# Kernel optimization log

Hardware: AMD Instinct MI355X
Metric: run time of the kernel (lower is better)

The kernel has to match this reference:

```python
import jax, jax.numpy as jnp
import numpy as np

B, NJ, NM = 64, 30, 20
N = NJ * NM          # 600 operation nodes per FJSP instance
IN_DIM, H = 2, 128


def _bn(h):
    # torch BatchNorm1d in training mode, gamma=1/beta=0 (module init), stats over all nodes
    m = h.mean(axis=(0, 1))
    v = h.var(axis=(0, 1))
    return (h - m) / jnp.sqrt(v + 1e-5)


def setup_inputs() -> dict:
    key = jax.random.key(0)
    ks = jax.random.split(key, 20)
    x = jax.random.normal(ks[0], (B, N, IN_DIM), jnp.float32)
    graph_pool = jnp.full((B, N), 1.0 / N, jnp.float32)   # average graph pooling weights
    padded_nei = jnp.zeros((1,), jnp.int32)               # unused (sum pooling path)
    adj = (jax.random.uniform(ks[1], (B, N, N)) < 0.01).astype(jnp.float32)
    adj = jnp.minimum(adj + jnp.eye(N, dtype=jnp.float32)[None], 1.0)  # self-loops
    candidate = jax.random.randint(ks[2], (B, NJ), 0, N)
    a_index = jax.random.randint(ks[3], (B,), 0, NJ)
    mask = jax.random.uniform(ks[4], (B, NJ)) < 0.2
    mask = mask.at[jnp.arange(B), a_index].set(False)     # chosen action never masked
    mask_mch = jax.random.uniform(ks[5], (B, N, NM)) < 0.3
    dur = jax.random.uniform(ks[6], (B, N, NM), dtype=jnp.float32)
    old_action = jax.random.randint(ks[7], (B,), 0, N)
    mch_pool = jax.random.normal(ks[8], (B, H), jnp.float32)

    def w(k, i, o):
        return jax.random.normal(k, (i, o), jnp.float32) * (1.0 / np.sqrt(i))

    z = lambda n: jnp.zeros((n,), jnp.float32)            # biases init to 0 in module
    return dict(
        x=x, graph_pool=graph_pool, padded_nei=padded_nei, adj=adj,
        candidate=candidate, mask=mask, mask_mch=mask_mch, dur=dur,
        a_index=a_index, old_action=old_action, mch_pool=mch_pool,
        W1_0=w(ks[9], IN_DIM, H), b1_0=z(H), W2_0=w(ks[10], H, H), b2_0=z(H),
        W1_1=w(ks[11], H, H), b1_1=z(H), W2_1=w(ks[12], H, H), b2_1=z(H),
        Wa1=w(ks[13], 3 * H, H), ba1=z(H), Wa2=w(ks[14], H, H), ba2=z(H),
        Wa3=w(ks[15], H, 1), ba3=z(1),
        Wc1=w(ks[16], H, H), bc1=z(H), Wc2=w(ks[17], H, 1), bc2=z(1),
    )


def reference(x, graph_pool, padded_nei, adj, candidate, mask, mask_mch, dur,
              a_index, old_action, mch_pool,
              W1_0, b1_0, W2_0, b2_0, W1_1, b1_1, W2_1, b2_1,
              Wa1, ba1, Wa2, ba2, Wa3, ba3, Wc1, bc1, Wc2, bc2):
    # --- GIN encoder: num_layers-1 = 2 message-passing layers, sum pooling ---
    h = x
    for (W1, b1, W2, b2) in ((W1_0, b1_0, W2_0, b2_0), (W1_1, b1_1, W2_1, b2_1)):
        pooled = jnp.einsum('bnm,bmd->bnd', adj, h)         # neighbor sum (adj has self-loops)
        h1 = jax.nn.relu(_bn(pooled @ W1 + b1))             # MLP hidden (BN inside MLP)
        h = jax.nn.relu(_bn(h1 @ W2 + b2))                  # layer BN + relu
    h_nodes = h                                             # [B, N, H]
    h_pooled = jnp.einsum('bn,bnd->bd', graph_pool, h_nodes)  # [B, H]

    # --- gather candidate features, concat pooled contexts ---
    cand_feat = jnp.take_along_axis(h_nodes, candidate[:, :, None], axis=1)  # [B, NJ, H]
    concat = jnp.concatenate([
        cand_feat,
        jnp.broadcast_to(h_pooled[:, None, :], cand_feat.shape),
        jnp.broadcast_to(mch_pool[:, None, :], cand_feat.shape)], axis=-1)   # [B, NJ, 3H]

    # --- MLPActor(3 layers, tanh) ---
    a = jnp.tanh(concat @ Wa1 + ba1)
    a = jnp.tanh(a @ Wa2 + ba2)
    scores = (a @ Wa3 + ba3).squeeze(-1) * 10.0             # [B, NJ]
    scores = jnp.where(mask, -jnp.inf, scores)
    logpi = jax.nn.log_softmax(scores, axis=1)
    pi = jnp.exp(logpi)
    log_a = jnp.take_along_axis(logpi, a_index[:, None], axis=1)[:, 0]
    entropy = -jnp.sum(jnp.where(pi > 0, pi * logpi, 0.0), axis=1)

    # --- gather action-dependent tensors (detached in torch) ---
    b_idx = jnp.arange(B)
    action_node = dur[b_idx, old_action]                    # [B, NM]
    action_feature = h_nodes[b_idx, old_action]             # [B, H]
    mask_mch_action = mask_mch[b_idx, old_action][:, None, :]  # [B, 1, NM]

    # --- MLPCritic(2 layers, tanh) ---
    v = jnp.tanh(h_pooled @ Wc1 + bc1) @ Wc2 + bc2          # [B, 1]

    sg = jax.lax.stop_gradient
    return (entropy, v, log_a, sg(action_node), sg(action_feature),
            mask_mch_action, sg(h_pooled))
```

## Files before the change

### kernel.cpp

```cpp
#include <hip/hip_runtime.h>
#include <hip/hip_bf16.h>

#define BB 64
#define NJ 30
#define NM 20
#define NN 600
#define HH 128
#define NROWS (BB*NN)
#define CAP 48

typedef __attribute__((ext_vector_type(8))) short short8;
typedef __attribute__((ext_vector_type(4))) float f32x4;

#define STATS_B   0
#define HPOOL_B   4096
#define FLAGS_B   36864
#define ZERO_B    36880
#define WTB_B     37120
#define SCORES_B  135424
#define NBRCNT_B  143104
#define NBRIDX_B  296704
#define POOLED0_B 7669504
#define T1_B      7976704
#define P1_B      27637504

#define OUT_ENT   0
#define OUT_V     64
#define OUT_LOGA  128
#define OUT_ANODE 192
#define OUT_AFEAT 1472
#define OUT_MMCH  9664
#define OUT_HPOOL 10944

__device__ __forceinline__ bool mask_at(const void* p, int layout, long i) {
    if (layout == 2) return ((const float*)p)[i] != 0.f;
    if (layout == 1) return ((const unsigned char*)p)[i] != 0;
    return ((const int*)p)[i] != 0;
}

__device__ __forceinline__ short bf16rne(float f) {
    unsigned u = __float_as_uint(f);
    return (short)((u + 0x7fffu + ((u >> 16) & 1u)) >> 16);
}
__device__ __forceinline__ float bf2f(unsigned h) {
    return __uint_as_float(h << 16);
}
__device__ __forceinline__ unsigned packbf(float a, float b) {
    return ((unsigned)(unsigned short)bf16rne(a)) |
           (((unsigned)(unsigned short)bf16rne(b)) << 16);
}

__global__ __launch_bounds__(256) void k_detect(const void* mask_p, const void* maskmch_p,
                                                int* flags) {
    unsigned agg = 0;
    int which;
    int tid = threadIdx.x;
    if (blockIdx.x == 0) {
        which = 0;
        const unsigned* p = (const unsigned*)mask_p;
        unsigned w0 = (tid < 480) ? p[tid] : 0u;
        unsigned w1 = (tid + 256 < 480) ? p[tid + 256] : 0u;
        agg = w0 | w1;
    } else {
        which = 1;
        const unsigned* p = (const unsigned*)maskmch_p + (size_t)(blockIdx.x - 1) * 800;
        unsigned w0 = p[tid];
        unsigned w1 = (tid + 256 < 800) ? p[tid + 256] : 0u;
        unsigned w2 = (tid + 512 < 800) ? p[tid + 512] : 0u;
        unsigned w3 = (tid + 768 < 800) ? p[tid + 768] : 0u;
        agg = w0 | w1 | w2 | w3;
    }
    int f = 0;
    if (((agg >> 24) & 0xffu) == 0x3fu) f |= 1;
    if ((((agg >> 8) & 0xffu) == 1u) || (((agg >> 16) & 0xffu) == 1u) ||
        (((agg >> 24) & 0xffu) == 1u)) f |= 2;
#pragma unroll
    for (int off = 1; off < 64; off <<= 1) f |= __shfl_xor(f, off);
    if ((tid & 63) == 0 && f) atomicOr(&flags[which], f);
}

__global__ void k_wconv(const float* __restrict__ Wa, const float* __restrict__ Wb,
                        const float* __restrict__ Wc, unsigned short* __restrict__ wT) {
    int mat = blockIdx.x >> 6;
    int idx = ((blockIdx.x & 63) << 8) + threadIdx.x;
    const float* W = mat == 0 ? Wa : (mat == 1 ? Wb : Wc);
    int k = idx >> 7, c = idx & 127;
    wT[mat * 16384 + c * HH + k] = (unsigned short)bf16rne(W[idx]);
}

__global__ __launch_bounds__(256) void k_sparse(const float* __restrict__ adj,
                                                const float* __restrict__ x,
                                                int* __restrict__ nbr_cnt,
                                                int* __restrict__ nbr_idx,
                                                float* __restrict__ pooled0) {
    int wrow = blockIdx.x * 4 + (threadIdx.x >> 6);
    int lane = threadIdx.x & 63;
    int b = wrow / NN;
    const float4* arow = (const float4*)(adj + (size_t)wrow * NN);
    int* irow = nbr_idx + (size_t)wrow * CAP;
    const float* xb = x + (size_t)b * NN * 2;
    float4 vv[3];
    vv[0] = arow[lane];
    vv[1] = arow[64 + lane];
    vv[2] = (128 + lane < 150) ? arow[128 + lane] : make_float4(0.f, 0.f, 0.f, 0.f);
    int cnt = 0;
    float p0 = 0.f, p1 = 0.f;
#pragma unroll
    for (int it = 0; it < 3; ++it) {
        int fi = it * 64 + lane;
#pragma unroll
        for (int s = 0; s < 4; ++s) {
            float c = s == 0 ? vv[it].x : (s == 1 ? vv[it].y : (s == 2 ? vv[it].z : vv[it].w));
            bool pred = (c != 0.f);
            unsigned long long bal = __ballot(pred);
            if (pred) {
                int pos = cnt + __popcll(bal & ((1ull << lane) - 1ull));
                int m = fi * 4 + s;
                if (pos < CAP) irow[pos] = m;
                float2 xv = *(const float2*)&xb[m * 2];
                p0 += xv.x; p1 += xv.y;
            }
            cnt += __popcll(bal);
        }
    }
#pragma unroll
    for (int off = 1; off < 64; off <<= 1) {
        p0 += __shfl_xor(p0, off);
        p1 += __shfl_xor(p1, off);
    }
    if (lane == 0) {
        nbr_cnt[wrow] = cnt < CAP ? cnt : CAP;
        pooled0[(size_t)wrow * 2]     = p0;
        pooled0[(size_t)wrow * 2 + 1] = p1;
    }
}

__global__ __launch_bounds__(256) void k_p0stats(const float* __restrict__ pooled0,
                                                 float* __restrict__ out5) {
    __shared__ float red[4][5];
    int i = blockIdx.x * 256 + threadIdx.x;
    float p0 = pooled0[(size_t)i * 2], p1 = pooled0[(size_t)i * 2 + 1];
    float v[5] = {p0, p1, p0 * p0, p1 * p1, p0 * p1};
#pragma unroll
    for (int j = 0; j < 5; ++j)
#pragma unroll
        for (int off = 1; off < 64; off <<= 1) v[j] += __shfl_xor(v[j], off);
    int lane = threadIdx.x & 63, w = threadIdx.x >> 6;
    if (lane == 0)
#pragma unroll
        for (int j = 0; j < 5; ++j) red[w][j] = v[j];
    __syncthreads();
    if (threadIdx.x == 0)
#pragma unroll
        for (int j = 0; j < 5; ++j)
            atomicAdd(&out5[j], red[0][j] + red[1][j] + red[2][j] + red[3][j]);
}

template<int MODE>
__global__ __launch_bounds__(256) void k_stage(const void* __restrict__ t_in_v,
                                               const float* __restrict__ pooled0,
                                               const float* __restrict__ W1,
                                               const unsigned short* __restrict__ wT,
                                               const float* __restrict__ stats_in,
                                               unsigned short* __restrict__ t_out,
                                               float* __restrict__ stats_out) {
    __shared__ float sm_mean[HH], sm_inv[HH];
    __shared__ float smS[4][HH], smQ[4][HH];
    int tid = threadIdx.x;
    if (MODE == 0 && tid < HH) {
        float S0 = stats_in[0], S1 = stats_in[1], Q0 = stats_in[2], Q1 = stats_in[3], P01 = stats_in[4];
        float w0 = W1[tid], w1 = W1[HH + tid];
        float m = (S0 * w0 + S1 * w1) * (1.f / NROWS);
        float eq = (Q0 * w0 * w0 + Q1 * w1 * w1 + 2.f * P01 * w0 * w1) * (1.f / NROWS);
        sm_mean[tid] = m;
        sm_inv[tid] = 1.f / sqrtf(eq - m * m + 1e-5f);
    }
    if (MODE == 1 && tid < HH) {
        float s = stats_in[tid], q = stats_in[HH + tid];
        float m = s * (1.f / NROWS);
        sm_mean[tid] = m;
        sm_inv[tid] = 1.f / sqrtf(q * (1.f / NROWS) - m * m + 1e-5f);
    }
    if (MODE != 2) __syncthreads();

    const unsigned short* tin = (const unsigned short*)t_in_v;
    int lane = tid & 63, wave = tid >> 6;
    int r16 = lane & 15, kg = lane >> 4;
    int rowbase = blockIdx.x * 64 + wave * 16;

    f32x4 acc[8];
#pragma unroll
    for (int t = 0; t < 8; ++t)
#pragma unroll
        for (int i = 0; i < 4; ++i) acc[t][i] = 0.f;

    float p0 = 0.f, p1 = 0.f;
    if (MODE == 0) {
        p0 = pooled0[(size_t)(rowbase + r16) * 2];
        p1 = pooled0[(size_t)(rowbase + r16) * 2 + 1];
    }

#pragma unroll
    for (int ks = 0; ks < 4; ++ks) {
        int kb = ks * 32 + kg * 8;
        short8 afr;
        if (MODE == 2) {
            afr = *(const short8*)&tin[(size_t)(rowbase + r16) * HH + kb];
        } else {
            float av[8];
            if (MODE == 0) {
                float4 wa0 = *(const float4*)&W1[kb];
                float4 wa1 = *(const float4*)&W1[kb + 4];
                float4 wb0 = *(const float4*)&W1[HH + kb];
                float4 wb1 = *(const float4*)&W1[HH + kb + 4];
                av[0] = p0 * wa0.x + p1 * wb0.x; av[1] = p0 * wa0.y + p1 * wb0.y;
                av[2] = p0 * wa0.z + p1 * wb0.z; av[3] = p0 * wa0.w + p1 * wb0.w;
                av[4] = p0 * wa1.x + p1 * wb1.x; av[5] = p0 * wa1.y + p1 * wb1.y;
                av[6] = p0 * wa1.z + p1 * wb1.z; av[7] = p0 * wa1.w + p1 * wb1.w;
            } else {
                short8 raw = *(const short8*)&tin[(size_t)(rowbase + r16) * HH + kb];
#pragma unroll
                for (int j = 0; j < 8; ++j) av[j] = bf2f((unsigned short)raw[j]);
            }
            float4 m0 = *(const float4*)&sm_mean[kb];
            float4 m1 = *(const float4*)&sm_mean[kb + 4];
            float4 i0 = *(const float4*)&sm_inv[kb];
            float4 i1 = *(const float4*)&sm_inv[kb + 4];
            av[0] = fmaxf((av[0] - m0.x) * i0.x, 0.f);
            av[1] = fmaxf((av[1] - m0.y) * i0.y, 0.f);
            av[2] = fmaxf((av[2] - m0.z) * i0.z, 0.f);
            av[3] = fmaxf((av[3] - m0.w) * i0.w, 0.f);
            av[4] = fmaxf((av[4] - m1.x) * i1.x, 0.f);
            av[5] = fmaxf((av[5] - m1.y) * i1.y, 0.f);
            av[6] = fmaxf((av[6] - m1.z) * i1.z, 0.f);
            av[7] = fmaxf((av[7] - m1.w) * i1.w, 0.f);
#pragma unroll
            for (int j = 0; j < 8; ++j) afr[j] = bf16rne(av[j]);
        }
#pragma unroll
        for (int t = 0; t < 8; ++t) {
            short8 bfr = *(const short8*)&wT[(size_t)(t * 16 + r16) * HH + kb];
            acc[t] = __builtin_amdgcn_mfma_f32_16x16x32_bf16(afr, bfr, acc[t], 0, 0, 0);
        }
    }

#pragma unroll
    for (int t = 0; t < 8; ++t) {
        int col = t * 16 + r16;
        float s = 0.f, q = 0.f;
#pragma unroll
        for (int i = 0; i < 4; ++i) {
            float v = acc[t][i];
            t_out[(size_t)(rowbase + kg * 4 + i) * HH + col] = (unsigned short)bf16rne(v);
            s += v; q += v * v;
        }
        s += __shfl_xor(s, 16); q += __shfl_xor(q, 16);
        s += __shfl_xor(s, 32); q += __shfl_xor(q, 32);
        if (kg == 0) { smS[wave][col] = s; smQ[wave][col] = q; }
    }
    __syncthreads();
    if (tid < HH) {
        atomicAdd(&stats_out[tid],      smS[0][tid] + smS[1][tid] + smS[2][tid] + smS[3][tid]);
        atomicAdd(&stats_out[HH + tid], smQ[0][tid] + smQ[1][tid] + smQ[2][tid] + smQ[3][tid]);
    }
}

__global__ __launch_bounds__(256) void k_pool1(const unsigned short* __restrict__ t1,
                                               const int* __restrict__ nbr_cnt,
                                               const int* __restrict__ nbr_idx,
                                               const float* __restrict__ stats1,
                                               unsigned short* __restrict__ pooled1) {
    __shared__ float sm_mean[HH], sm_inv[HH];
    int tid = threadIdx.x;
    if (tid < HH) {
        float s = stats1[tid], q = stats1[HH + tid];
        float m = s * (1.f / NROWS);
        sm_mean[tid] = m;
        sm_inv[tid] = 1.f / sqrtf(q * (1.f / NROWS) - m * m + 1e-5f);
    }
    __syncthreads();
    int c4 = tid & 31, rl = tid >> 5;
    int row = blockIdx.x * 8 + rl;
    int b = row / NN;
    float4 mm = *(const float4*)&sm_mean[c4 * 4];
    float4 iv = *(const float4*)&sm_inv[c4 * 4];
    int cnt = nbr_cnt[row];
    const int* ir = nbr_idx + (size_t)row * CAP;
    const unsigned short* tb = t1 + (size_t)b * NN * HH;
    float a0 = 0.f, a1 = 0.f, a2 = 0.f, a3 = 0.f;
    int i = 0;
    for (; i + 1 < cnt; i += 2) {
        int m0 = ir[i], m1 = ir[i + 1];
        uint2 w0 = *(const uint2*)&tb[(size_t)m0 * HH + c4 * 4];
        uint2 w1 = *(const uint2*)&tb[(size_t)m1 * HH + c4 * 4];
        a0 += fmaxf((bf2f(w0.x & 0xffffu) - mm.x) * iv.x, 0.f)
            + fmaxf((bf2f(w1.x & 0xffffu) - mm.x) * iv.x, 0.f);
        a1 += fmaxf((bf2f(w0.x >> 16)     - mm.y) * iv.y, 0.f)
            + fmaxf((bf2f(w1.x >> 16)     - mm.y) * iv.y, 0.f);
        a2 += fmaxf((bf2f(w0.y & 0xffffu) - mm.z) * iv.z, 0.f)
            + fmaxf((bf2f(w1.y & 0xffffu) - mm.z) * iv.z, 0.f);
        a3 += fmaxf((bf2f(w0.y >> 16)     - mm.w) * iv.w, 0.f)
            + fmaxf((bf2f(w1.y >> 16)     - mm.w) * iv.w, 0.f);
    }
    if (i < cnt) {
        int m0 = ir[i];
        uint2 w0 = *(const uint2*)&tb[(size_t)m0 * HH + c4 * 4];
        a0 += fmaxf((bf2f(w0.x & 0xffffu) - mm.x) * iv.x, 0.f);
        a1 += fmaxf((bf2f(w0.x >> 16)     - mm.y) * iv.y, 0.f);
        a2 += fmaxf((bf2f(w0.y & 0xffffu) - mm.z) * iv.z, 0.f);
        a3 += fmaxf((bf2f(w0.y >> 16)     - mm.w) * iv.w, 0.f);
    }
    uint2 o;
    o.x = packbf(a0, a1);
    o.y = packbf(a2, a3);
    *(uint2*)&pooled1[(size_t)row * HH + c4 * 4] = o;
}

__global__ __launch_bounds__(256) void k_hpool(const unsigned short* __restrict__ t3,
                                               const float* __restrict__ gp,
                                               const float* __restrict__ stats3,
                                               float* __restrict__ hpool) {
    __shared__ float sm_mean[HH], sm_inv[HH];
    __shared__ float red[256];
    int tid = threadIdx.x;
    if (tid < HH) {
        float s = stats3[tid], q = stats3[HH + tid];
        float m = s * (1.f / NROWS);
        sm_mean[tid] = m;
        sm_inv[tid] = 1.f / sqrtf(q * (1.f / NROWS) - m * m + 1e-5f);
    }
    __syncthreads();
    int b = blockIdx.x >> 3, chunk = blockIdx.x & 7;
    int c = tid & 127, rr = tid >> 7;
    float m = sm_mean[c], iv = sm_inv[c];
    float acc = 0.f;
    for (int n = chunk * 75 + rr; n < chunk * 75 + 75; n += 2) {
        float w = gp[b * NN + n];
        float v = bf2f(t3[((size_t)b * NN + n) * HH + c]);
        acc += w * fmaxf((v - m) * iv, 0.f);
    }
    red[tid] = acc;
    __syncthreads();
    if (tid < HH) atomicAdd(&hpool[b * HH + c], red[c] + red[c + 128]);
}

__global__ __launch_bounds__(256) void k_actor(const unsigned short* __restrict__ t3,
                                               const int* __restrict__ cand,
                                               const float* __restrict__ hpool,
                                               const float* __restrict__ mch,
                                               const float* __restrict__ stats3,
                                               const float* __restrict__ Wa1,
                                               const float* __restrict__ ba1,
                                               const float* __restrict__ Wa2,
                                               const float* __restrict__ ba2,
                                               const float* __restrict__ Wa3,
                                               const float* __restrict__ ba3,
                                               float* __restrict__ scores) {
    __shared__ float sh_c[8 * 384];
    __shared__ float sh_a1[8 * HH];
    __shared__ float sred[8][HH];
    int tid = threadIdx.x;
    int rbase = blockIdx.x * 8;
    int c = tid & 127, slot = tid >> 7;

    float mean_c, inv_c;
    {
        float s = stats3[c], q = stats3[HH + c];
        float m = s * (1.f / NROWS);
        mean_c = m;
        inv_c = 1.f / sqrtf(q * (1.f / NROWS) - m * m + 1e-5f);
    }
#pragma unroll
    for (int rr = 0; rr < 4; ++rr) {
        int r = slot * 4 + rr;
        int row = rbase + r;
        int b = row / NJ;
        int cd = cand[row];
        float v = bf2f(t3[((size_t)b * NN + cd) * HH + c]);
        sh_c[r * 384 + c]       = fmaxf((v - mean_c) * inv_c, 0.f);
        sh_c[r * 384 + 128 + c] = hpool[b * HH + c];
        sh_c[r * 384 + 256 + c] = mch[b * HH + c];
    }
    __syncthreads();

    float acc[4] = {0.f, 0.f, 0.f, 0.f};
    for (int k = 0; k < 384; ++k) {
        float w = Wa1[(size_t)k * HH + c];
#pragma unroll
        for (int rr = 0; rr < 4; ++rr)
            acc[rr] += sh_c[(slot * 4 + rr) * 384 + k] * w;
    }
    float bb = ba1[c];
#pragma unroll
    for (int rr = 0; rr < 4; ++rr)
        sh_a1[(slot * 4 + rr) * HH + c] = tanhf(acc[rr] + bb);
    __syncthreads();

    float acc2[4] = {0.f, 0.f, 0.f, 0.f};
    for (int k = 0; k < HH; ++k) {
        float w = Wa2[(size_t)k * HH + c];
#pragma unroll
        for (int rr = 0; rr < 4; ++rr)
            acc2[rr] += sh_a1[(slot * 4 + rr) * HH + k] * w;
    }
    float w3 = Wa3[c], bb2 = ba2[c];
#pragma unroll
    for (int rr = 0; rr < 4; ++rr)
        sred[slot * 4 + rr][c] = tanhf(acc2[rr] + bb2) * w3;
    __syncthreads();
    int r = tid >> 5, l32 = tid & 31;
    float v = sred[r][l32] + sred[r][l32 + 32] + sred[r][l32 + 64] + sred[r][l32 + 96];
    v += __shfl_xor(v, 1); v += __shfl_xor(v, 2); v += __shfl_xor(v, 4);
    v += __shfl_xor(v, 8); v += __shfl_xor(v, 16);
    if (l32 == 0) scores[rbase + r] = 10.f * (v + ba3[0]);
}

__global__ __launch_bounds__(128) void k_final(const unsigned short* __restrict__ t3,
                                               const float* __restrict__ stats3,
                                               const float* __restrict__ hpool,
                                               const float* __restrict__ scores,
                                               const void* __restrict__ mask_p,
                                               const void* __restrict__ maskmch_p,
                                               const int* __restrict__ flags,
                                               const float* __restrict__ dur,
                                               const int* __restrict__ a_index,
                                               const int* __restrict__ old_action,
                                               const float* __restrict__ Wc1,
                                               const float* __restrict__ bc1,
                                               const float* __restrict__ Wc2,
                                               const float* __restrict__ bc2,
                                               float* __restrict__ out) {
    __shared__ float sm_mean[HH], sm_inv[HH], sh_hp[HH], sh_red[HH];
    __shared__ float sh_s[32], sh_lp[32];
    __shared__ int sh_m[32];
    int b = blockIdx.x, t = threadIdx.x;
    {
        float s = stats3[t], q = stats3[HH + t];
        float m = s * (1.f / NROWS);
        sm_mean[t] = m;
        sm_inv[t] = 1.f / sqrtf(q * (1.f / NROWS) - m * m + 1e-5f);
    }
    sh_hp[t] = hpool[b * HH + t];
    __syncthreads();

    float acc = bc1[t];
    for (int k = 0; k < HH; ++k) acc += sh_hp[k] * Wc1[k * HH + t];
    sh_red[t] = tanhf(acc) * Wc2[t];
    __syncthreads();
    for (int st = 64; st > 0; st >>= 1) {
        if (t < st) sh_red[t] += sh_red[t + st];
        __syncthreads();
    }
    if (t == 0) out[OUT_V + b] = sh_red[0] + bc2[0];

    int fA = flags[0], fB = flags[1];
    int layA = (fA & 1) ? 2 : ((fA & 2) ? 1 : 0);
    int layB = (fB & 1) ? 2 : ((fB & 2) ? 1 : 0);
    if (t < NJ) {
        sh_s[t] = scores[b * NJ + t];
        sh_m[t] = mask_at(mask_p, layA, (long)b * NJ + t) ? 1 : 0;
    }
    __syncthreads();
    if (t == 0) {
        float mx = -1e30f;
        for (int j = 0; j < NJ; ++j)
            if (!sh_m[j] && sh_s[j] > mx) mx = sh_s[j];
        float sum = 0.f;
        for (int j = 0; j < NJ; ++j)
            if (!sh_m[j]) sum += expf(sh_s[j] - mx);
        float lse = mx + logf(sum);
        float ent = 0.f;
        for (int j = 0; j < NJ; ++j) {
            if (!sh_m[j]) {
                float lp = sh_s[j] - lse;
                sh_lp[j] = lp;
                float pi = expf(lp);
                if (pi > 0.f) ent -= pi * lp;
            }
        }
        out[OUT_ENT + b] = ent;
        out[OUT_LOGA + b] = sh_lp[a_index[b]];
    }

    int old = old_action[b];
    if (t < NM) {
        out[OUT_ANODE + b * NM + t] = dur[((size_t)b * NN + old) * NM + t];
        out[OUT_MMCH + b * NM + t] =
            mask_at(maskmch_p, layB, ((size_t)b * NN + old) * NM + t) ? 1.f : 0.f;
    }
    {
        float v = bf2f(t3[((size_t)b * NN + old) * HH + t]);
        out[OUT_AFEAT + b * HH + t] = fmaxf((v - sm_mean[t]) * sm_inv[t], 0.f);
        out[OUT_HPOOL + b * HH + t] = sh_hp[t];
    }
}

extern "C" void kernel_launch(void* const* d_in, const int* in_sizes, int n_in,
                              void* d_out, int out_size, void* d_ws, size_t ws_size,
                              hipStream_t stream) {
    (void)in_sizes; (void)n_in; (void)out_size; (void)ws_size;
    const float* x         = (const float*)d_in[0];
    const float* gp        = (const float*)d_in[1];
    const float* adj       = (const float*)d_in[3];
    const int*   cand      = (const int*)d_in[4];
    const void*  mask_p    = d_in[5];
    const void*  maskmch_p = d_in[6];
    const float* dur       = (const float*)d_in[7];
    const int*   a_index   = (const int*)d_in[8];
    const int*   old_act   = (const int*)d_in[9];
    const float* mch_pool  = (const float*)d_in[10];
    const float* W1_0 = (const float*)d_in[11];
    const float* W2_0 = (const float*)d_in[13];
    const float* W1_1 = (const float*)d_in[15];
    const float* W2_1 = (const float*)d_in[17];
    const float* Wa1  = (const float*)d_in[19];
    const float* ba1  = (const float*)d_in[20];
    const float* Wa2  = (const float*)d_in[21];
    const float* ba2  = (const float*)d_in[22];
    const float* Wa3  = (const float*)d_in[23];
    const float* ba3  = (const float*)d_in[24];
    const float* Wc1  = (const float*)d_in[25];
    const float* bc1  = (const float*)d_in[26];
    const float* Wc2  = (const float*)d_in[27];
    const float* bc2  = (const float*)d_in[28];

    char* ws = (char*)d_ws;
    float* stats   = (float*)(ws + STATS_B);
    float* hpool   = (float*)(ws + HPOOL_B);
    int*   flags   = (int*)(ws + FLAGS_B);
    unsigned short* wtb = (unsigned short*)(ws + WTB_B);
    float* scores  = (float*)(ws + SCORES_B);
    int*   nbr_cnt = (int*)(ws + NBRCNT_B);
    int*   nbr_idx = (int*)(ws + NBRIDX_B);
    float* pooled0 = (float*)(ws + POOLED0_B);
    unsigned short* t1_16 = (unsigned short*)(ws + T1_B);
    unsigned short* p1_16 = (unsigned short*)(ws + P1_B);
    float* out     = (float*)d_out;

    hipMemsetAsync(ws, 0, ZERO_B, stream);
    k_detect<<<25, 256, 0, stream>>>(mask_p, maskmch_p, flags);
    k_wconv<<<192, 256, 0, stream>>>(W2_0, W1_1, W2_1, wtb);
    k_sparse<<<NROWS / 4, 256, 0, stream>>>(adj, x, nbr_cnt, nbr_idx, pooled0);
    k_p0stats<<<NROWS / 256, 256, 0, stream>>>(pooled0, stats);
    k_stage<0><<<600, 256, 0, stream>>>(nullptr, pooled0, W1_0, wtb, stats, t1_16, stats + 256);
    k_pool1<<<NROWS / 8, 256, 0, stream>>>(t1_16, nbr_cnt, nbr_idx, stats + 256, p1_16);
    k_stage<2><<<600, 256, 0, stream>>>(p1_16, nullptr, nullptr, wtb + 16384, stats, t1_16, stats + 512);
    k_stage<1><<<600, 256, 0, stream>>>(t1_16, nullptr, nullptr, wtb + 32768, stats + 512, p1_16, stats + 768);
    k_hpool<<<BB * 8, 256, 0, stream>>>(p1_16, gp, stats + 768, hpool);
    k_actor<<<240, 256, 0, stream>>>(p1_16, cand, hpool, mch_pool, stats + 768,
                                     Wa1, ba1, Wa2, ba2, Wa3, ba3, scores);
    k_a_unused_guard: ;
    k_final<<<BB, 128, 0, stream>>>(p1_16, stats + 768, hpool, scores, mask_p, maskmch_p, flags,
                                    dur, a_index, old_act, Wc1, bc1, Wc2, bc2, out);
}
```

Before: 379.9 us.

## Merge mask detection with weight conversion and vectorise sparse scan and pooling

Fuses the mask-layout detection and weight transpose/bf16 conversion into one launch, removing one kernel launch. The detect part now spreads mask_mch over 96 blocks of 200 words each instead of 24 blocks of 800. Rewrites the adjacency compaction to use one prefix scan per float4 instead of four ballots. It also vectorises the graph-pooling kernel to read four bf16 channels per thread with an 8-way row split. These cut launch overhead and per-element instruction count in small, mostly memory-bound kernels. Neighbour ordering inside each row changes from column-interleaved to lane-contiguous, which alters the order of the pooled sums.

Measured after the change: 368.4 us. 3.0% less time.

```diff
diff --git a/kernel.cpp b/kernel.cpp
--- a/kernel.cpp
+++ b/kernel.cpp
@@ -50,12 +50,26 @@
            (((unsigned)(unsigned short)bf16rne(b)) << 16);
 }
 
-__global__ __launch_bounds__(256) void k_detect(const void* mask_p, const void* maskmch_p,
-                                                int* flags) {
+__global__ __launch_bounds__(256) void k_pre(const void* mask_p, const void* maskmch_p,
+                                             int* flags,
+                                             const float* __restrict__ Wa,
+                                             const float* __restrict__ Wb,
+                                             const float* __restrict__ Wc,
+                                             unsigned short* __restrict__ wT) {
+    int bid = blockIdx.x;
+    int tid = threadIdx.x;
+    if (bid >= 97) {
+        int bid2 = bid - 97;
+        int mat = bid2 >> 6;
+        int idx = ((bid2 & 63) << 8) + tid;
+        const float* W = mat == 0 ? Wa : (mat == 1 ? Wb : Wc);
+        int k = idx >> 7, c = idx & 127;
+        wT[mat * 16384 + c * HH + k] = (unsigned short)bf16rne(W[idx]);
+        return;
+    }
     unsigned agg = 0;
     int which;
-    int tid = threadIdx.x;
-    if (blockIdx.x == 0) {
+    if (bid == 0) {
         which = 0;
         const unsigned* p = (const unsigned*)mask_p;
         unsigned w0 = (tid < 480) ? p[tid] : 0u;
@@ -63,12 +77,8 @@
         agg = w0 | w1;
     } else {
         which = 1;
-        const unsigned* p = (const unsigned*)maskmch_p + (size_t)(blockIdx.x - 1) * 800;
-        unsigned w0 = p[tid];
-        unsigned w1 = (tid + 256 < 800) ? p[tid + 256] : 0u;
-        unsigned w2 = (tid + 512 < 800) ? p[tid + 512] : 0u;
-        unsigned w3 = (tid + 768 < 800) ? p[tid + 768] : 0u;
-        agg = w0 | w1 | w2 | w3;
+        const unsigned* p = (const unsigned*)maskmch_p + (size_t)(bid - 1) * 200;
+        agg = (tid < 200) ? p[tid] : 0u;
     }
     int f = 0;
     if (((agg >> 24) & 0xffu) == 0x3fu) f |= 1;
@@ -77,15 +87,6 @@
 #pragma unroll
     for (int off = 1; off < 64; off <<= 1) f |= __shfl_xor(f, off);
     if ((tid & 63) == 0 && f) atomicOr(&flags[which], f);
-}
-
-__global__ void k_wconv(const float* __restrict__ Wa, const float* __restrict__ Wb,
-                        const float* __restrict__ Wc, unsigned short* __restrict__ wT) {
-    int mat = blockIdx.x >> 6;
-    int idx = ((blockIdx.x & 63) << 8) + threadIdx.x;
-    const float* W = mat == 0 ? Wa : (mat == 1 ? Wb : Wc);
-    int k = idx >> 7, c = idx & 127;
-    wT[mat * 16384 + c * HH + k] = (unsigned short)bf16rne(W[idx]);
 }
 
 __global__ __launch_bounds__(256) void k_sparse(const float* __restrict__ adj,
@@ -107,21 +108,38 @@
     float p0 = 0.f, p1 = 0.f;
 #pragma unroll
     for (int it = 0; it < 3; ++it) {
-        int fi = it * 64 + lane;
-#pragma unroll
-        for (int s = 0; s < 4; ++s) {
-            float c = s == 0 ? vv[it].x : (s == 1 ? vv[it].y : (s == 2 ? vv[it].z : vv[it].w));
-            bool pred = (c != 0.f);
-            unsigned long long bal = __ballot(pred);
-            if (pred) {
-                int pos = cnt + __popcll(bal & ((1ull << lane) - 1ull));
-                int m = fi * 4 + s;
-                if (pos < CAP) irow[pos] = m;
-                float2 xv = *(const float2*)&xb[m * 2];
-                p0 += xv.x; p1 += xv.y;
-            }
-            cnt += __popcll(bal);
-        }
+        float4 v = vv[it];
+        int col0 = it * 256 + lane * 4;
+        bool m0 = v.x != 0.f, m1 = v.y != 0.f, m2 = v.z != 0.f, m3 = v.w != 0.f;
+        int c_lane = (int)m0 + (int)m1 + (int)m2 + (int)m3;
+        int inc = c_lane;
+#pragma unroll
+        for (int off = 1; off < 64; off <<= 1) {
+            int t = __shfl_up(inc, off);
+            if (lane >= off) inc += t;
+        }
+        int pos = cnt + inc - c_lane;
+        if (m0) {
+            if (pos < CAP) irow[pos] = col0;
+            float2 xv = *(const float2*)&xb[col0 * 2];
+            p0 += xv.x; p1 += xv.y; ++pos;
+        }
+        if (m1) {
+            if (pos < CAP) irow[pos] = col0 + 1;
+            float2 xv = *(const float2*)&xb[(col0 + 1) * 2];
+            p0 += xv.x; p1 += xv.y; ++pos;
+        }
+        if (m2) {
+            if (pos < CAP) irow[pos] = col0 + 2;
+            float2 xv = *(const float2*)&xb[(col0 + 2) * 2];
+            p0 += xv.x; p1 += xv.y; ++pos;
+        }
+        if (m3) {
+            if (pos < CAP) irow[pos] = col0 + 3;
+            float2 xv = *(const float2*)&xb[(col0 + 3) * 2];
+            p0 += xv.x; p1 += xv.y; ++pos;
+        }
+        cnt += __shfl(inc, 63);
     }
 #pragma unroll
     for (int off = 1; off < 64; off <<= 1) {
@@ -321,7 +339,7 @@
                                                const float* __restrict__ stats3,
                                                float* __restrict__ hpool) {
     __shared__ float sm_mean[HH], sm_inv[HH];
-    __shared__ float red[256];
+    __shared__ float red[8][HH];
     int tid = threadIdx.x;
     if (tid < HH) {
         float s = stats3[tid], q = stats3[HH + tid];
@@ -331,17 +349,27 @@
     }
     __syncthreads();
     int b = blockIdx.x >> 3, chunk = blockIdx.x & 7;
-    int c = tid & 127, rr = tid >> 7;
-    float m = sm_mean[c], iv = sm_inv[c];
-    float acc = 0.f;
-    for (int n = chunk * 75 + rr; n < chunk * 75 + 75; n += 2) {
+    int c4 = tid & 31, rl = tid >> 5;
+    float4 mm = *(const float4*)&sm_mean[c4 * 4];
+    float4 iv = *(const float4*)&sm_inv[c4 * 4];
+    float a0 = 0.f, a1 = 0.f, a2 = 0.f, a3 = 0.f;
+    int nend = chunk * 75 + 75;
+    for (int n = chunk * 75 + rl; n < nend; n += 8) {
         float w = gp[b * NN + n];
-        float v = bf2f(t3[((size_t)b * NN + n) * HH + c]);
-        acc += w * fmaxf((v - m) * iv, 0.f);
-    }
-    red[tid] = acc;
-    __syncthreads();
-    if (tid < HH) atomicAdd(&hpool[b * HH + c], red[c] + red[c + 128]);
+        uint2 t = *(const uint2*)&t3[((size_t)b * NN + n) * HH + c4 * 4];
+        a0 += w * fmaxf((bf2f(t.x & 0xffffu) - mm.x) * iv.x, 0.f);
+        a1 += w * fmaxf((bf2f(t.x >> 16)     - mm.y) * iv.y, 0.f);
+        a2 += w * fmaxf((bf2f(t.y & 0xffffu) - mm.z) * iv.z, 0.f);
+        a3 += w * fmaxf((bf2f(t.y >> 16)     - mm.w) * iv.w, 0.f);
+    }
+    *(float4*)&red[rl][c4 * 4] = make_float4(a0, a1, a2, a3);
+    __syncthreads();
+    if (tid < HH) {
+        float s = 0.f;
+#pragma unroll
+        for (int g = 0; g < 8; ++g) s += red[g][tid];
+        atomicAdd(&hpool[b * HH + tid], s);
+    }
 }
 
 __global__ __launch_bounds__(256) void k_actor(const unsigned short* __restrict__ t3,
@@ -538,8 +566,7 @@
     float* out     = (float*)d_out;
 
     hipMemsetAsync(ws, 0, ZERO_B, stream);
-    k_detect<<<25, 256, 0, stream>>>(mask_p, maskmch_p, flags);
-    k_wconv<<<192, 256, 0, stream>>>(W2_0, W1_1, W2_1, wtb);
+    k_pre<<<289, 256, 0, stream>>>(mask_p, maskmch_p, flags, W2_0, W1_1, W2_1, wtb);
     k_sparse<<<NROWS / 4, 256, 0, stream>>>(adj, x, nbr_cnt, nbr_idx, pooled0);
     k_p0stats<<<NROWS / 256, 256, 0, stream>>>(pooled0, stats);
     k_stage<0><<<600, 256, 0, stream>>>(nullptr, pooled0, W1_0, wtb, stats, t1_16, stats + 256);
@@ -549,7 +576,6 @@
     k_hpool<<<BB * 8, 256, 0, stream>>>(p1_16, gp, stats + 768, hpool);
     k_actor<<<240, 256, 0, stream>>>(p1_16, cand, hpool, mch_pool, stats + 768,
                                      Wa1, ba1, Wa2, ba2, Wa3, ba3, scores);
-    k_a_unused_guard: ;
     k_final<<<BB, 128, 0, stream>>>(p1_16, stats + 768, hpool, scores, mask_p, maskmch_p, flags,
                                     dur, a_index, old_act, Wc1, bc1, Wc2, bc2, out);
 }
```
